# Kernel optimization log

Hardware: AMD Instinct MI355X
Metric: run time of the kernel (lower is better)

## Reference

```python
import jax, jax.numpy as jnp
import numpy as np

B, CIN, H, W = 4, 256, 64, 64
COUT = CIN // 2  # 128
EPS = 1e-5


def setup_inputs() -> dict:
    key = jax.random.key(0)
    ks = jax.random.split(key, 10)
    s_in = 1.0 / np.sqrt(CIN)
    s_out = 1.0 / np.sqrt(COUT)
    return {
        "x": jax.random.normal(ks[0], (B, CIN, H, W), dtype=jnp.float32),
        "Wq": jax.random.uniform(ks[1], (COUT, CIN), jnp.float32, -s_in, s_in),
        "bq": jax.random.uniform(ks[2], (COUT,), jnp.float32, -s_in, s_in),
        "Wk": jax.random.uniform(ks[3], (COUT, CIN), jnp.float32, -s_in, s_in),
        "bk": jax.random.uniform(ks[4], (COUT,), jnp.float32, -s_in, s_in),
        "Wv": jax.random.uniform(ks[5], (COUT, CIN), jnp.float32, -s_in, s_in),
        "bv": jax.random.uniform(ks[6], (COUT,), jnp.float32, -s_in, s_in),
        "Ww": jax.random.uniform(ks[7], (CIN, COUT), jnp.float32, -s_out, s_out),
        "bw": jax.random.uniform(ks[8], (CIN,), jnp.float32, -s_out, s_out),
        "bn_gamma": jnp.ones((CIN,), jnp.float32),
        "bn_beta": jnp.zeros((CIN,), jnp.float32),
        "bn_mean": jnp.zeros((CIN,), jnp.float32),
        "bn_var": jnp.ones((CIN,), jnp.float32),
    }


def reference(x, Wq, bq, Wk, bk, Wv, bv, Ww, bw, bn_gamma, bn_beta, bn_mean, bn_var):
    b, c, h, w = x.shape
    n = h * w
    xf = x.reshape(b, c, n)  # [B, Cin, N]
    # 1x1 convs == channel-mixing matmuls on flattened spatial dim
    q = jnp.einsum("oc,bcn->bon", Wq, xf) + bq[None, :, None]  # [B, Cout, N]
    k = jnp.einsum("oc,bcn->bon", Wk, xf) + bk[None, :, None]
    v = jnp.einsum("oc,bcn->bon", Wv, xf) + bv[None, :, None]
    # f = k^T @ q  (no scaling, as in the original)
    f = jnp.einsum("bcn,bcm->bnm", k, q)  # [B, N, N]
    f = jax.nn.softmax(f, axis=-1)
    # y = v @ f
    y = jnp.einsum("bcn,bnm->bcm", v, f)  # [B, Cout, N]
    # output 1x1 conv + eval-mode BatchNorm + residual
    z = jnp.einsum("oc,bcn->bon", Ww, y) + bw[None, :, None]  # [B, Cin, N]
    inv = bn_gamma / jnp.sqrt(bn_var + EPS)
    z = z * inv[None, :, None] + (bn_beta - bn_mean * inv)[None, :, None]
    return z.reshape(b, c, h, w) + x
```

## Files before the change

### kernel.cpp

```cpp
#include <hip/hip_runtime.h>
#include <hip/hip_bf16.h>

#define BATCH 4
#define CIN   256
#define CMID  128
#define NPOS  4096
#define EPS   1e-5f

typedef __bf16 bf16;
typedef __attribute__((ext_vector_type(8))) __bf16 bf16x8;
typedef __attribute__((ext_vector_type(4))) __bf16 bf16x4;
typedef __attribute__((ext_vector_type(4))) float  f32x4;

#define MFMA16(a, b, c) __builtin_amdgcn_mfma_f32_16x16x32_bf16((a), (b), (c), 0, 0, 0)

__device__ __forceinline__ int swz128(int row, int colb) {
    return row * 128 + ((((colb >> 4) ^ (row & 7)) << 4) | (colb & 15));
}
__device__ __forceinline__ int swz256(int row, int colb) {
    return row * 256 + ((((colb >> 4) ^ (row & 7)) << 4) | (colb & 15));
}

__global__ __launch_bounds__(256) void kt_transpose(const float* __restrict__ x,
                                                    bf16* __restrict__ xT) {
    __shared__ float tile[64][65];
    int n0 = blockIdx.x * 64, c0 = blockIdx.y * 64, b = blockIdx.z;
    const float* xp = x + (size_t)b * CIN * NPOS;
    int t = threadIdx.x;
    int lr = t >> 4;
    int lc4 = (t & 15) * 4;
    for (int p = 0; p < 4; ++p) {
        int c = lr + p * 16;
        f32x4 v = *reinterpret_cast<const f32x4*>(xp + (size_t)(c0 + c) * NPOS + n0 + lc4);
        tile[c][lc4 + 0] = v[0]; tile[c][lc4 + 1] = v[1];
        tile[c][lc4 + 2] = v[2]; tile[c][lc4 + 3] = v[3];
    }
    __syncthreads();
    bf16* xtp = xT + (size_t)b * NPOS * CIN;
    int cc = (t & 15) * 4;
    for (int p = 0; p < 4; ++p) {
        int n = (t >> 4) + p * 16;
        bf16x4 o;
        o[0] = (bf16)tile[cc + 0][n]; o[1] = (bf16)tile[cc + 1][n];
        o[2] = (bf16)tile[cc + 2][n]; o[3] = (bf16)tile[cc + 3][n];
        *reinterpret_cast<bf16x4*>(xtp + (size_t)(n0 + n) * CIN + c0 + cc) = o;
    }
}

__global__ __launch_bounds__(256) void k_qkv(
    const float* __restrict__ Wq, const float* __restrict__ Wk, const float* __restrict__ Wv,
    const float* __restrict__ bq, const float* __restrict__ bk, const float* __restrict__ bv,
    const bf16* __restrict__ xT, bf16* __restrict__ qT, bf16* __restrict__ kT,
    bf16* __restrict__ vC) {
    __shared__ __align__(16) char a_lds[128 * 128];
    __shared__ __align__(16) char b_lds[128 * 128];
    int n0 = blockIdx.x * 128, which = blockIdx.y, b = blockIdx.z;
    const float* W    = which == 0 ? Wq : (which == 1 ? Wk : Wv);
    const float* bias = which == 0 ? bq : (which == 1 ? bk : bv);
    int t = threadIdx.x, lane = t & 63, w = t >> 6, wy = w >> 1, wx = w & 1;
    const bf16* xb = xT + (size_t)b * NPOS * CIN;

    f32x4 acc[4][4] = {};
    for (int k0 = 0; k0 < 256; k0 += 64) {
        __syncthreads();
        for (int i = 0; i < 8; ++i) {
            int idx = t + i * 256;
            int row = idx >> 4, c4 = (idx & 15) * 4;
            f32x4 v = *reinterpret_cast<const f32x4*>(W + (size_t)row * CIN + k0 + c4);
            bf16x4 o; o[0] = (bf16)v[0]; o[1] = (bf16)v[1]; o[2] = (bf16)v[2]; o[3] = (bf16)v[3];
            *reinterpret_cast<bf16x4*>(a_lds + swz128(row, c4 * 2)) = o;
        }
        for (int i = 0; i < 4; ++i) {
            int idx = t + i * 256;
            int row = idx >> 3, cb = (idx & 7) * 16;
            bf16x8 vv = *reinterpret_cast<const bf16x8*>(xb + (size_t)(n0 + row) * CIN + k0 + cb / 2);
            *reinterpret_cast<bf16x8*>(b_lds + swz128(row, cb)) = vv;
        }
        __syncthreads();
        for (int ks = 0; ks < 2; ++ks) {
            int kb = ks * 64 + (lane >> 4) * 16;
            bf16x8 af[4], bfr[4];
            for (int i = 0; i < 4; ++i)
                af[i] = *reinterpret_cast<const bf16x8*>(a_lds + swz128(wy * 64 + i * 16 + (lane & 15), kb));
            for (int j = 0; j < 4; ++j)
                bfr[j] = *reinterpret_cast<const bf16x8*>(b_lds + swz128(wx * 64 + j * 16 + (lane & 15), kb));
            for (int i = 0; i < 4; ++i)
                for (int j = 0; j < 4; ++j)
                    acc[i][j] = MFMA16(af[i], bfr[j], acc[i][j]);
        }
    }
    int rg = lane >> 4, cl = lane & 15;
    for (int i = 0; i < 4; ++i) {
        int ch0 = wy * 64 + i * 16 + rg * 4;
        f32x4 bv4 = *reinterpret_cast<const f32x4*>(bias + ch0);
        for (int j = 0; j < 4; ++j) {
            int n = n0 + wx * 64 + j * 16 + cl;
            f32x4 d = acc[i][j];
            for (int r = 0; r < 4; ++r) d[r] += bv4[r];
            if (which == 2) {
                for (int r = 0; r < 4; ++r)
                    vC[((size_t)b * CMID + ch0 + r) * NPOS + n] = (bf16)d[r];
            } else {
                bf16x4 o; o[0] = (bf16)d[0]; o[1] = (bf16)d[1]; o[2] = (bf16)d[2]; o[3] = (bf16)d[3];
                bf16* dst = (which == 0 ? qT : kT);
                *reinterpret_cast<bf16x4*>(dst + ((size_t)b * NPOS + n) * CMID + ch0) = o;
            }
        }
    }
}

__global__ __launch_bounds__(256, 4) void k_zrow(const bf16* __restrict__ qT,
                                                 const bf16* __restrict__ kT,
                                                 float* __restrict__ zpart) {
    __shared__ __align__(16) char q_lds[64 * 256];
    int n0 = blockIdx.x * 128, mq = blockIdx.y, b = blockIdx.z;
    int t = threadIdx.x, lane = t & 63, w = t >> 6;
    int cl = lane & 15, g = lane >> 4;
    const bf16* qb = qT + (size_t)b * NPOS * CMID;
    const bf16* kb = kT + (size_t)b * NPOS * CMID;
    bf16x8 kreg[2][4];
    for (int jn = 0; jn < 2; ++jn)
        for (int ks = 0; ks < 4; ++ks)
            kreg[jn][ks] = *reinterpret_cast<const bf16x8*>(
                kb + (size_t)(n0 + w * 32 + jn * 16 + cl) * CMID + ks * 32 + g * 8);
    float zacc[2] = {0.f, 0.f};
    int mbeg = mq * (NPOS / 8);
    for (int m0 = mbeg; m0 < mbeg + NPOS / 8; m0 += 64) {
        __syncthreads();
        for (int i = 0; i < 4; ++i) {
            int idx = t + i * 256, row = idx >> 4, cb = (idx & 15) * 16;
            bf16x8 vv = *reinterpret_cast<const bf16x8*>(qb + (size_t)(m0 + row) * CMID + cb / 2);
            *reinterpret_cast<bf16x8*>(q_lds + swz256(row, cb)) = vv;
        }
        __syncthreads();
        f32x4 acc[4][2] = {};
        for (int ks = 0; ks < 4; ++ks) {
            bf16x8 qf[4];
            for (int im = 0; im < 4; ++im)
                qf[im] = *reinterpret_cast<const bf16x8*>(q_lds + swz256(im * 16 + cl, ks * 64 + g * 16));
            for (int im = 0; im < 4; ++im)
                for (int jn = 0; jn < 2; ++jn)
                    acc[im][jn] = MFMA16(qf[im], kreg[jn][ks], acc[im][jn]);
        }
        for (int im = 0; im < 4; ++im)
            for (int jn = 0; jn < 2; ++jn)
                for (int r = 0; r < 4; ++r)
                    zacc[jn] += __expf(acc[im][jn][r]);
    }
    for (int jn = 0; jn < 2; ++jn) {
        zacc[jn] += __shfl_xor(zacc[jn], 16);
        zacc[jn] += __shfl_xor(zacc[jn], 32);
    }
    if (g == 0) {
        float* zp = zpart + ((size_t)mq * BATCH + b) * NPOS;
        zp[n0 + w * 32 + cl]      = zacc[0];
        zp[n0 + w * 32 + 16 + cl] = zacc[1];
    }
}

__global__ __launch_bounds__(256) void k_rcp(const float* __restrict__ zpart,
                                             float* __restrict__ invZ) {
    int i = (blockIdx.x * 256 + threadIdx.x) * 4;
    f32x4 s = {0.f, 0.f, 0.f, 0.f};
    for (int p = 0; p < 8; ++p) {
        f32x4 a = *reinterpret_cast<const f32x4*>(zpart + (size_t)p * BATCH * NPOS + i);
        for (int r = 0; r < 4; ++r) s[r] += a[r];
    }
    f32x4 o;
    for (int r = 0; r < 4; ++r) o[r] = 1.f / s[r];
    *reinterpret_cast<f32x4*>(invZ + i) = o;
}

__global__ __launch_bounds__(256, 2) void k_attn(const bf16* __restrict__ qT,
                                                 const bf16* __restrict__ kT,
                                                 const bf16* __restrict__ vC,
                                                 const float* __restrict__ invZ,
                                                 bf16* __restrict__ ypA,
                                                 bf16* __restrict__ ypB) {
    __shared__ __align__(16) char k_lds[64 * 256];
    __shared__ __align__(16) char v_lds[128 * 128];
    __shared__ __align__(16) char p_lds[128 * 128];
    int m0 = blockIdx.x * 128, nq = blockIdx.y, b = blockIdx.z;
    int t = threadIdx.x, lane = t & 63, w = t >> 6;
    int cl = lane & 15, g = lane >> 4;
    const bf16* qb = qT + (size_t)b * NPOS * CMID;
    const bf16* kb = kT + (size_t)b * NPOS * CMID;
    const bf16* vb = vC + (size_t)b * CMID * NPOS;
    const float* izb = invZ + (size_t)b * NPOS;
    bf16x8 qreg[2][4];
    for (int jm = 0; jm < 2; ++jm)
        for (int ks = 0; ks < 4; ++ks)
            qreg[jm][ks] = *reinterpret_cast<const bf16x8*>(
                qb + (size_t)(m0 + w * 32 + jm * 16 + cl) * CMID + ks * 32 + g * 8);

    f32x4 acc2[8][2] = {};
    int nbeg = nq * (NPOS / 4);
    for (int n0 = nbeg; n0 < nbeg + NPOS / 4; n0 += 64) {
        __syncthreads();
        for (int i = 0; i < 4; ++i) {
            int idx = t + i * 256, row = idx >> 4, cb = (idx & 15) * 16;
            bf16x8 vv = *reinterpret_cast<const bf16x8*>(kb + (size_t)(n0 + row) * CMID + cb / 2);
            *reinterpret_cast<bf16x8*>(k_lds + swz256(row, cb)) = vv;
        }
        for (int i = 0; i < 4; ++i) {
            int idx = t + i * 256, row = idx >> 3, cb = (idx & 7) * 16;
            bf16x8 vv = *reinterpret_cast<const bf16x8*>(vb + (size_t)row * NPOS + n0 + cb / 2);
            *reinterpret_cast<bf16x8*>(v_lds + swz128(row, cb)) = vv;
        }
        __syncthreads();
        f32x4 acc1[4][2] = {};
        for (int ks = 0; ks < 4; ++ks) {
            bf16x8 kf[4];
            for (int in = 0; in < 4; ++in)
                kf[in] = *reinterpret_cast<const bf16x8*>(k_lds + swz256(in * 16 + cl, ks * 64 + g * 16));
            for (int in = 0; in < 4; ++in)
                for (int jm = 0; jm < 2; ++jm)
                    acc1[in][jm] = MFMA16(kf[in], qreg[jm][ks], acc1[in][jm]);
        }
        for (int in = 0; in < 4; ++in) {
            f32x4 iz = *reinterpret_cast<const f32x4*>(izb + n0 + in * 16 + g * 4);
            for (int jm = 0; jm < 2; ++jm) {
                bf16x4 o;
                for (int r = 0; r < 4; ++r) o[r] = (bf16)(__expf(acc1[in][jm][r]) * iz[r]);
                *reinterpret_cast<bf16x4*>(p_lds + swz128(w * 32 + jm * 16 + cl, in * 32 + g * 8)) = o;
            }
        }
        __syncthreads();
        for (int ks = 0; ks < 2; ++ks) {
            bf16x8 af[8], vf[2];
            for (int i = 0; i < 8; ++i)
                af[i] = *reinterpret_cast<const bf16x8*>(p_lds + swz128(i * 16 + cl, ks * 64 + g * 16));
            for (int j = 0; j < 2; ++j)
                vf[j] = *reinterpret_cast<const bf16x8*>(v_lds + swz128(w * 32 + j * 16 + cl, ks * 64 + g * 16));
            for (int i = 0; i < 8; ++i)
                for (int j = 0; j < 2; ++j)
                    acc2[i][j] = MFMA16(af[i], vf[j], acc2[i][j]);
        }
    }
    bf16* yb = ((nq & 2) ? ypB : ypA) + ((size_t)(nq & 1) * BATCH + b) * NPOS * CMID
             + (size_t)m0 * CMID;
    for (int i = 0; i < 8; ++i)
        for (int j = 0; j < 2; ++j) {
            int c = w * 32 + j * 16 + cl;
            for (int r = 0; r < 4; ++r) {
                int m = i * 16 + g * 4 + r;
                yb[(size_t)m * CMID + c] = (bf16)acc2[i][j][r];
            }
        }
}

__global__ __launch_bounds__(256) void k_out(
    const float* __restrict__ Ww, const float* __restrict__ bw,
    const float* __restrict__ gamma, const float* __restrict__ beta,
    const float* __restrict__ mean, const float* __restrict__ var,
    const bf16* __restrict__ ypA, const bf16* __restrict__ ypB,
    const float* __restrict__ x, float* __restrict__ out) {
    __shared__ __align__(16) char a_lds[128 * 128];
    __shared__ __align__(16) char b_lds[128 * 128];
    int m0 = blockIdx.x * 128, o0 = blockIdx.y * 128, b = blockIdx.z;
    int t = threadIdx.x, lane = t & 63, w = t >> 6, wy = w >> 1, wx = w & 1;
    size_t boff = (size_t)b * NPOS * CMID;
    const bf16* y0 = ypA + boff;
    const bf16* y1 = ypA + (size_t)BATCH * NPOS * CMID + boff;
    const bf16* y2 = ypB + boff;
    const bf16* y3 = ypB + (size_t)BATCH * NPOS * CMID + boff;
    f32x4 acc[4][4] = {};
    for (int k0 = 0; k0 < 128; k0 += 64) {
        __syncthreads();
        for (int i = 0; i < 8; ++i) {
            int idx = t + i * 256, row = idx >> 4, c4 = (idx & 15) * 4;
            f32x4 v = *reinterpret_cast<const f32x4*>(Ww + (size_t)(o0 + row) * CMID + k0 + c4);
            bf16x4 o; o[0] = (bf16)v[0]; o[1] = (bf16)v[1]; o[2] = (bf16)v[2]; o[3] = (bf16)v[3];
            *reinterpret_cast<bf16x4*>(a_lds + swz128(row, c4 * 2)) = o;
        }
        for (int i = 0; i < 8; ++i) {
            int idx = t + i * 256, row = idx >> 4, c4 = (idx & 15) * 4;
            size_t yoff = (size_t)(m0 + row) * CMID + k0 + c4;
            bf16x4 a0 = *reinterpret_cast<const bf16x4*>(y0 + yoff);
            bf16x4 a1 = *reinterpret_cast<const bf16x4*>(y1 + yoff);
            bf16x4 a2 = *reinterpret_cast<const bf16x4*>(y2 + yoff);
            bf16x4 a3 = *reinterpret_cast<const bf16x4*>(y3 + yoff);
            bf16x4 o;
            for (int r = 0; r < 4; ++r)
                o[r] = (bf16)((float)a0[r] + (float)a1[r] + (float)a2[r] + (float)a3[r]);
            *reinterpret_cast<bf16x4*>(b_lds + swz128(row, c4 * 2)) = o;
        }
        __syncthreads();
        for (int ks = 0; ks < 2; ++ks) {
            int kb = ks * 64 + (lane >> 4) * 16;
            bf16x8 af[4], bfr[4];
            for (int i = 0; i < 4; ++i)
                af[i] = *reinterpret_cast<const bf16x8*>(a_lds + swz128(wy * 64 + i * 16 + (lane & 15), kb));
            for (int j = 0; j < 4; ++j)
                bfr[j] = *reinterpret_cast<const bf16x8*>(b_lds + swz128(wx * 64 + j * 16 + (lane & 15), kb));
            for (int i = 0; i < 4; ++i)
                for (int j = 0; j < 4; ++j)
                    acc[i][j] = MFMA16(af[i], bfr[j], acc[i][j]);
        }
    }
    int rg = lane >> 4, cl = lane & 15;
    const float* xb = x + (size_t)b * CIN * NPOS;
    float* ob = out + (size_t)b * CIN * NPOS;
    for (int i = 0; i < 4; ++i) {
        int och0 = o0 + wy * 64 + i * 16 + rg * 4;
        f32x4 g  = *reinterpret_cast<const f32x4*>(gamma + och0);
        f32x4 be = *reinterpret_cast<const f32x4*>(beta + och0);
        f32x4 mu = *reinterpret_cast<const f32x4*>(mean + och0);
        f32x4 va = *reinterpret_cast<const f32x4*>(var + och0);
        f32x4 bb = *reinterpret_cast<const f32x4*>(bw + och0);
        float invv[4], addv[4];
        for (int r = 0; r < 4; ++r) {
            invv[r] = g[r] / sqrtf(va[r] + EPS);
            addv[r] = be[r] - mu[r] * invv[r];
        }
        for (int j = 0; j < 4; ++j) {
            int m = m0 + wx * 64 + j * 16 + cl;
            for (int r = 0; r < 4; ++r) {
                float z = (acc[i][j][r] + bb[r]) * invv[r] + addv[r];
                ob[(size_t)(och0 + r) * NPOS + m] = z + xb[(size_t)(och0 + r) * NPOS + m];
            }
        }
    }
}

extern "C" void kernel_launch(void* const* d_in, const int* in_sizes, int n_in,
                              void* d_out, int out_size, void* d_ws, size_t ws_size,
                              hipStream_t stream) {
    const float* x     = (const float*)d_in[0];
    const float* Wq    = (const float*)d_in[1];
    const float* bq    = (const float*)d_in[2];
    const float* Wk    = (const float*)d_in[3];
    const float* bk    = (const float*)d_in[4];
    const float* Wv    = (const float*)d_in[5];
    const float* bv    = (const float*)d_in[6];
    const float* Ww    = (const float*)d_in[7];
    const float* bw    = (const float*)d_in[8];
    const float* gamma = (const float*)d_in[9];
    const float* beta  = (const float*)d_in[10];
    const float* mean  = (const float*)d_in[11];
    const float* var   = (const float*)d_in[12];
    float* out = (float*)d_out;

    char* ws = (char*)d_ws;
    char* regionA = ws;                    ws += (size_t)BATCH * NPOS * CIN * 2;
    bf16* qT = (bf16*)ws;                  ws += (size_t)BATCH * NPOS * CMID * 2;
    bf16* kT = (bf16*)ws;                  ws += (size_t)BATCH * NPOS * CMID * 2;
    bf16* vC = (bf16*)ws;                  ws += (size_t)BATCH * NPOS * CMID * 2;
    bf16* ypB = (bf16*)ws;                 ws += (size_t)2 * BATCH * NPOS * CMID * 2;
    float* zpart = (float*)ws;             ws += (size_t)8 * BATCH * NPOS * 4;
    float* invZ = (float*)ws;
    bf16* xT  = (bf16*)regionA;
    bf16* ypA = (bf16*)regionA;

    kt_transpose<<<dim3(NPOS / 64, CIN / 64, BATCH), 256, 0, stream>>>(x, xT);
    k_qkv<<<dim3(NPOS / 128, 3, BATCH), 256, 0, stream>>>(Wq, Wk, Wv, bq, bk, bv, xT, qT, kT, vC);
    k_zrow<<<dim3(NPOS / 128, 8, BATCH), 256, 0, stream>>>(qT, kT, zpart);
    k_rcp<<<dim3(BATCH * NPOS / 1024), 256, 0, stream>>>(zpart, invZ);
    k_attn<<<dim3(NPOS / 128, 4, BATCH), 256, 0, stream>>>(qT, kT, vC, invZ, ypA, ypB);
    k_out<<<dim3(NPOS / 128, 2, BATCH), 256, 0, stream>>>(Ww, bw, gamma, beta, mean, var, ypA, ypB, x, out);
}
```

Before: 101.3 us.

## Double-buffer Q/K/V tiles with async global-to-LDS loads in zrow and attention kernels

Both the softmax-denominator kernel and the attention kernel now prefetch the next K/V (or Q) tile into a second LDS buffer. They use `global_load_lds` direct copies with the XOR swizzle applied on the global address side, so the copy overlaps the current tile's MFMA and exp work, and one barrier per iteration is removed. The invZ loads are also hoisted ahead of the first matmul. In exchange, LDS use doubles for the staged tiles (80KB per attention block), which may limit occupancy. Correctness relies on the end-of-loop barrier also waiting on the outstanding async loads.

```diff
diff --git a/kernel.cpp b/kernel.cpp
--- a/kernel.cpp
+++ b/kernel.cpp
@@ -13,6 +13,11 @@
 typedef __attribute__((ext_vector_type(4))) float  f32x4;
 
 #define MFMA16(a, b, c) __builtin_amdgcn_mfma_f32_16x16x32_bf16((a), (b), (c), 0, 0, 0)
+
+#define GLDS(gsrc, ldst) \
+    __builtin_amdgcn_global_load_lds( \
+        (const __attribute__((address_space(1))) void*)(gsrc), \
+        (__attribute__((address_space(3))) void*)(ldst), 16, 0, 0)
 
 __device__ __forceinline__ int swz128(int row, int colb) {
     return row * 128 + ((((colb >> 4) ^ (row & 7)) << 4) | (colb & 15));
@@ -112,32 +117,42 @@
 __global__ __launch_bounds__(256, 4) void k_zrow(const bf16* __restrict__ qT,
                                                  const bf16* __restrict__ kT,
                                                  float* __restrict__ zpart) {
-    __shared__ __align__(16) char q_lds[64 * 256];
+    __shared__ __align__(16) char q_lds[2][64 * 256];
     int n0 = blockIdx.x * 128, mq = blockIdx.y, b = blockIdx.z;
     int t = threadIdx.x, lane = t & 63, w = t >> 6;
     int cl = lane & 15, g = lane >> 4;
     const bf16* qb = qT + (size_t)b * NPOS * CMID;
     const bf16* kb = kT + (size_t)b * NPOS * CMID;
+
+    auto stage_q = [&](int buf, int m0) {
+        #pragma unroll
+        for (int i = 0; i < 4; ++i) {
+            int lc = (w * 4 + i) * 64 + lane;
+            int r = lc >> 4, p = lc & 15;
+            GLDS(qb + (size_t)(m0 + r) * CMID + ((p ^ (r & 7)) << 3),
+                 q_lds[buf] + (w * 4 + i) * 1024);
+        }
+    };
+
     bf16x8 kreg[2][4];
     for (int jn = 0; jn < 2; ++jn)
         for (int ks = 0; ks < 4; ++ks)
             kreg[jn][ks] = *reinterpret_cast<const bf16x8*>(
                 kb + (size_t)(n0 + w * 32 + jn * 16 + cl) * CMID + ks * 32 + g * 8);
+
+    int mbeg = mq * (NPOS / 8);
+    stage_q(0, mbeg);
+    asm volatile("s_waitcnt vmcnt(0)" ::: "memory");
+    __syncthreads();
+    int cur = 0;
     float zacc[2] = {0.f, 0.f};
-    int mbeg = mq * (NPOS / 8);
     for (int m0 = mbeg; m0 < mbeg + NPOS / 8; m0 += 64) {
-        __syncthreads();
-        for (int i = 0; i < 4; ++i) {
-            int idx = t + i * 256, row = idx >> 4, cb = (idx & 15) * 16;
-            bf16x8 vv = *reinterpret_cast<const bf16x8*>(qb + (size_t)(m0 + row) * CMID + cb / 2);
-            *reinterpret_cast<bf16x8*>(q_lds + swz256(row, cb)) = vv;
-        }
-        __syncthreads();
+        if (m0 + 64 < mbeg + NPOS / 8) stage_q(cur ^ 1, m0 + 64);
         f32x4 acc[4][2] = {};
         for (int ks = 0; ks < 4; ++ks) {
             bf16x8 qf[4];
             for (int im = 0; im < 4; ++im)
-                qf[im] = *reinterpret_cast<const bf16x8*>(q_lds + swz256(im * 16 + cl, ks * 64 + g * 16));
+                qf[im] = *reinterpret_cast<const bf16x8*>(q_lds[cur] + swz256(im * 16 + cl, ks * 64 + g * 16));
             for (int im = 0; im < 4; ++im)
                 for (int jn = 0; jn < 2; ++jn)
                     acc[im][jn] = MFMA16(qf[im], kreg[jn][ks], acc[im][jn]);
@@ -146,6 +161,8 @@
             for (int jn = 0; jn < 2; ++jn)
                 for (int r = 0; r < 4; ++r)
                     zacc[jn] += __expf(acc[im][jn][r]);
+        __syncthreads();
+        cur ^= 1;
     }
     for (int jn = 0; jn < 2; ++jn) {
         zacc[jn] += __shfl_xor(zacc[jn], 16);
@@ -177,8 +194,8 @@
                                                  const float* __restrict__ invZ,
                                                  bf16* __restrict__ ypA,
                                                  bf16* __restrict__ ypB) {
-    __shared__ __align__(16) char k_lds[64 * 256];
-    __shared__ __align__(16) char v_lds[128 * 128];
+    __shared__ __align__(16) char k_lds[2][64 * 256];
+    __shared__ __align__(16) char v_lds[2][128 * 128];
     __shared__ __align__(16) char p_lds[128 * 128];
     int m0 = blockIdx.x * 128, nq = blockIdx.y, b = blockIdx.z;
     int t = threadIdx.x, lane = t & 63, w = t >> 6;
@@ -187,6 +204,20 @@
     const bf16* kb = kT + (size_t)b * NPOS * CMID;
     const bf16* vb = vC + (size_t)b * CMID * NPOS;
     const float* izb = invZ + (size_t)b * NPOS;
+
+    auto stage_kv = [&](int buf, int n0) {
+        #pragma unroll
+        for (int i = 0; i < 4; ++i) {
+            int lc = (w * 4 + i) * 64 + lane;
+            int kr = lc >> 4, kp = lc & 15;
+            GLDS(kb + (size_t)(n0 + kr) * CMID + ((kp ^ (kr & 7)) << 3),
+                 k_lds[buf] + (w * 4 + i) * 1024);
+            int vr = lc >> 3, vp = lc & 7;
+            GLDS(vb + (size_t)vr * NPOS + n0 + ((vp ^ (vr & 7)) << 3),
+                 v_lds[buf] + (w * 4 + i) * 1024);
+        }
+    };
+
     bf16x8 qreg[2][4];
     for (int jm = 0; jm < 2; ++jm)
         for (int ks = 0; ks < 4; ++ks)
@@ -195,47 +226,44 @@
 
     f32x4 acc2[8][2] = {};
     int nbeg = nq * (NPOS / 4);
-    for (int n0 = nbeg; n0 < nbeg + NPOS / 4; n0 += 64) {
-        __syncthreads();
-        for (int i = 0; i < 4; ++i) {
-            int idx = t + i * 256, row = idx >> 4, cb = (idx & 15) * 16;
-            bf16x8 vv = *reinterpret_cast<const bf16x8*>(kb + (size_t)(n0 + row) * CMID + cb / 2);
-            *reinterpret_cast<bf16x8*>(k_lds + swz256(row, cb)) = vv;
-        }
-        for (int i = 0; i < 4; ++i) {
-            int idx = t + i * 256, row = idx >> 3, cb = (idx & 7) * 16;
-            bf16x8 vv = *reinterpret_cast<const bf16x8*>(vb + (size_t)row * NPOS + n0 + cb / 2);
-            *reinterpret_cast<bf16x8*>(v_lds + swz128(row, cb)) = vv;
-        }
-        __syncthreads();
+    stage_kv(0, nbeg);
+    asm volatile("s_waitcnt vmcnt(0)" ::: "memory");
+    __syncthreads();
+    int cur = 0;
+    for (int s = 0; s < NPOS / 4 / 64; ++s) {
+        int n0 = nbeg + s * 64;
+        if (s + 1 < NPOS / 4 / 64) stage_kv(cur ^ 1, n0 + 64);
+        f32x4 iz[4];
+        for (int in = 0; in < 4; ++in)
+            iz[in] = *reinterpret_cast<const f32x4*>(izb + n0 + in * 16 + g * 4);
         f32x4 acc1[4][2] = {};
         for (int ks = 0; ks < 4; ++ks) {
             bf16x8 kf[4];
             for (int in = 0; in < 4; ++in)
-                kf[in] = *reinterpret_cast<const bf16x8*>(k_lds + swz256(in * 16 + cl, ks * 64 + g * 16));
+                kf[in] = *reinterpret_cast<const bf16x8*>(k_lds[cur] + swz256(in * 16 + cl, ks * 64 + g * 16));
             for (int in = 0; in < 4; ++in)
                 for (int jm = 0; jm < 2; ++jm)
                     acc1[in][jm] = MFMA16(kf[in], qreg[jm][ks], acc1[in][jm]);
         }
-        for (int in = 0; in < 4; ++in) {
-            f32x4 iz = *reinterpret_cast<const f32x4*>(izb + n0 + in * 16 + g * 4);
+        for (int in = 0; in < 4; ++in)
             for (int jm = 0; jm < 2; ++jm) {
                 bf16x4 o;
-                for (int r = 0; r < 4; ++r) o[r] = (bf16)(__expf(acc1[in][jm][r]) * iz[r]);
+                for (int r = 0; r < 4; ++r) o[r] = (bf16)(__expf(acc1[in][jm][r]) * iz[in][r]);
                 *reinterpret_cast<bf16x4*>(p_lds + swz128(w * 32 + jm * 16 + cl, in * 32 + g * 8)) = o;
             }
-        }
         __syncthreads();
         for (int ks = 0; ks < 2; ++ks) {
             bf16x8 af[8], vf[2];
             for (int i = 0; i < 8; ++i)
                 af[i] = *reinterpret_cast<const bf16x8*>(p_lds + swz128(i * 16 + cl, ks * 64 + g * 16));
             for (int j = 0; j < 2; ++j)
-                vf[j] = *reinterpret_cast<const bf16x8*>(v_lds + swz128(w * 32 + j * 16 + cl, ks * 64 + g * 16));
+                vf[j] = *reinterpret_cast<const bf16x8*>(v_lds[cur] + swz128(w * 32 + j * 16 + cl, ks * 64 + g * 16));
             for (int i = 0; i < 8; ++i)
                 for (int j = 0; j < 2; ++j)
                     acc2[i][j] = MFMA16(af[i], vf[j], acc2[i][j]);
         }
+        __syncthreads();
+        cur ^= 1;
     }
     bf16* yb = ((nq & 2) ? ypB : ypA) + ((size_t)(nq & 1) * BATCH + b) * NPOS * CMID
              + (size_t)m0 * CMID;
```

After: 101.3 us. No clear change (-0.0%).
